# Kernel tuning notes

Measured on AMD Instinct MI355X. Metric: run time of the kernel, lower is better.

Reference implementation:

```python
import jax, jax.numpy as jnp
import numpy as np

HEADS = 4
ALPHA = 0.2  # leaky relu negative slope


def setup_inputs() -> dict:
    key = jax.random.key(0)
    ks = jax.random.split(key, 8)
    N, Fin, Fout = 4096, 512, 256
    return {
        "h": jax.random.normal(ks[0], (N, Fin), dtype=jnp.float32),
        "adj": jax.random.randint(ks[1], (N, N), 0, 2, dtype=jnp.int32),
        "W": jax.random.normal(ks[2], (Fin, Fout), dtype=jnp.float32) * (Fin ** -0.5),
        "Wl_w": jax.random.normal(ks[3], (Fout, Fout), dtype=jnp.float32) * (Fout ** -0.5),
        "Wl_b": jax.random.normal(ks[4], (Fout,), dtype=jnp.float32) * 0.02,
        "Wqkv_w": jax.random.normal(ks[5], (3 * Fout, Fout), dtype=jnp.float32) * (Fout ** -0.5),
        "Wqkv_b": jax.random.normal(ks[6], (3 * Fout,), dtype=jnp.float32) * 0.02,
        "a": jax.random.normal(ks[7], (2 * Fout, 1), dtype=jnp.float32) * (Fout ** -0.5),
    }


def reference(h, adj, W, Wl_w, Wl_b, Wqkv_w, Wqkv_b, a):
    N = h.shape[0]
    Fout = W.shape[1]
    d = Fout // HEADS
    scale = Fout ** -0.5  # note: original scales by out_features^-0.5, not head_dim

    Wh = h @ W                      # [N, Fout]
    Wh = Wh @ Wl_w.T + Wl_b         # to_linear

    qkv = Wh @ Wqkv_w.T + Wqkv_b    # [N, 3*Fout]
    q, k, v = jnp.split(qkv, 3, axis=-1)
    to_heads = lambda t: t.reshape(N, HEADS, d).transpose(1, 0, 2)  # [H, N, d]
    q, k, v = to_heads(q), to_heads(k), to_heads(v)

    dots = jax.nn.softmax(jnp.einsum('hid,hjd->hij', q, k) * scale, axis=-1)  # [H,N,N]
    Wh0 = jnp.einsum('hij,hjd->hid', dots, v)            # [H, N, d]
    Wh0 = Wh0.transpose(1, 0, 2).reshape(N, Fout)        # i (h d)
    Wh0 = jax.nn.softmax(Wh0, axis=-1)

    # GAT score decomposed: e_ij = leakyrelu(Wh_i . a1 + Wh_j . a2)
    a1 = a[:Fout, 0]
    a2 = a[Fout:, 0]
    e = jax.nn.leaky_relu((Wh @ a1)[:, None] + (Wh @ a2)[None, :], negative_slope=ALPHA)

    dsum = dots.sum(axis=0)                              # [N, N]
    neg = jnp.float32(-9e15)
    attention = jnp.where(adj > 0, e + dsum, neg)
    attention = jax.nn.softmax(attention, axis=1)
    # dropout p=0.0 / eval mode -> identity

    h_prime = attention @ Wh + Wh0
    return jax.nn.elu(h_prime)  # concat=True
```

## Files before the change

kernel.cpp:

```cpp
#include <hip/hip_runtime.h>

typedef float  f32x4 __attribute__((ext_vector_type(4)));
typedef short  s16x8 __attribute__((ext_vector_type(8)));
typedef unsigned short u16x8 __attribute__((ext_vector_type(8)));

#define NROWS 4096
#define ALPHA_LR 0.2f
#define SCALE 0.0625f

static __device__ __forceinline__ unsigned short bf16_rne(float x) {
    unsigned u = __float_as_uint(x);
    u += 0x7fffu + ((u >> 16) & 1u);
    return (unsigned short)(u >> 16);
}
static __device__ __forceinline__ unsigned short bf16_trunc(float x) {
    return (unsigned short)(__float_as_uint(x) >> 16);
}
static __device__ __forceinline__ float bf2f(unsigned short h) {
    return __uint_as_float(((unsigned)h) << 16);
}
static __device__ __forceinline__ float bflo(unsigned u) { return __uint_as_float(u << 16); }
static __device__ __forceinline__ float bfhi(unsigned u) { return __uint_as_float(u & 0xffff0000u); }
static __device__ __forceinline__ float wmax16(float v) {
#pragma unroll
    for (int o = 8; o; o >>= 1) v = fmaxf(v, __shfl_xor(v, o, 16));
    return v;
}
static __device__ __forceinline__ float wsum16(float v) {
#pragma unroll
    for (int o = 8; o; o >>= 1) v += __shfl_xor(v, o, 16);
    return v;
}

__global__ __launch_bounds__(256) void wprep(
    const float* __restrict__ W, const float* __restrict__ Wq,
    unsigned short* __restrict__ Whi, unsigned short* __restrict__ Wlo,
    unsigned short* __restrict__ Qhi, unsigned short* __restrict__ Qlo)
{
    int i = blockIdx.x * 256 + threadIdx.x;
    if (i < 131072) {
        float v = W[i];
        unsigned short hh = bf16_trunc(v);
        Whi[i] = hh; Wlo[i] = bf16_rne(v - bf2f(hh));
    }
    if (i < 196608) {
        float v = Wq[i];
        unsigned short hh = bf16_trunc(v);
        Qhi[i] = hh; Qlo[i] = bf16_rne(v - bf2f(hh));
    }
}

template <int EPI, bool BIAS>
__global__ __launch_bounds__(256) void gemm_mfma(
    const float* __restrict__ A,
    const unsigned short* __restrict__ Bhi, const unsigned short* __restrict__ Blo,
    const float* __restrict__ bias,
    float* __restrict__ C, unsigned short* __restrict__ o0,
    unsigned short* __restrict__ o1, unsigned short* __restrict__ o2,
    int M, int Nn, int K)
{
    __shared__ unsigned short Ah[64][40];
    __shared__ unsigned short Al[64][40];
    __shared__ unsigned short Bh[64][40];
    __shared__ unsigned short Bl[64][40];

    const int tid = threadIdx.x;
    const int w = tid >> 6;
    const int ln = tid & 63;
    const int l15 = ln & 15;
    const int lhi = ln >> 4;
    const int bm = blockIdx.y * 64;
    const int bn = blockIdx.x * 64;
    const int sm = tid >> 2;
    const int sk = (tid & 3) * 8;

    f32x4 acc[4];
#pragma unroll
    for (int cf = 0; cf < 4; ++cf) acc[cf] = (f32x4){0.f, 0.f, 0.f, 0.f};

    const float* arow = &A[(size_t)(bm + sm) * K];
    const unsigned short* bhrow = &Bhi[(size_t)(bn + sm) * K];
    const unsigned short* blrow = &Blo[(size_t)(bn + sm) * K];

    float4 a0r = *(const float4*)(arow + sk);
    float4 a1r = *(const float4*)(arow + sk + 4);
    uint4 bhr = *(const uint4*)(bhrow + sk);
    uint4 blr = *(const uint4*)(blrow + sk);

    for (int k0 = 0; k0 < K; k0 += 32) {
        float vv[8] = {a0r.x, a0r.y, a0r.z, a0r.w, a1r.x, a1r.y, a1r.z, a1r.w};
        unsigned hp[4], lp[4];
#pragma unroll
        for (int q = 0; q < 4; ++q) {
            unsigned short h0 = bf16_trunc(vv[q * 2]);
            unsigned short h1 = bf16_trunc(vv[q * 2 + 1]);
            unsigned short l0 = bf16_rne(vv[q * 2] - bf2f(h0));
            unsigned short l1 = bf16_rne(vv[q * 2 + 1] - bf2f(h1));
            hp[q] = (unsigned)h0 | ((unsigned)h1 << 16);
            lp[q] = (unsigned)l0 | ((unsigned)l1 << 16);
        }
        __syncthreads();
        *(uint4*)&Ah[sm][sk] = make_uint4(hp[0], hp[1], hp[2], hp[3]);
        *(uint4*)&Al[sm][sk] = make_uint4(lp[0], lp[1], lp[2], lp[3]);
        *(uint4*)&Bh[sm][sk] = bhr;
        *(uint4*)&Bl[sm][sk] = blr;
        const int kn = (k0 + 32 < K) ? k0 + 32 : 0;
        a0r = *(const float4*)(arow + kn + sk);
        a1r = *(const float4*)(arow + kn + sk + 4);
        bhr = *(const uint4*)(bhrow + kn + sk);
        blr = *(const uint4*)(blrow + kn + sk);
        __syncthreads();
        s16x8 ah = *(const s16x8*)&Ah[w * 16 + l15][lhi * 8];
        s16x8 al2 = *(const s16x8*)&Al[w * 16 + l15][lhi * 8];
        __builtin_amdgcn_s_setprio(1);
#pragma unroll
        for (int cf = 0; cf < 4; ++cf) {
            s16x8 bh = *(const s16x8*)&Bh[cf * 16 + l15][lhi * 8];
            s16x8 bl = *(const s16x8*)&Bl[cf * 16 + l15][lhi * 8];
            acc[cf] = __builtin_amdgcn_mfma_f32_16x16x32_bf16(ah, bh, acc[cf], 0, 0, 0);
            acc[cf] = __builtin_amdgcn_mfma_f32_16x16x32_bf16(ah, bl, acc[cf], 0, 0, 0);
            acc[cf] = __builtin_amdgcn_mfma_f32_16x16x32_bf16(al2, bh, acc[cf], 0, 0, 0);
        }
        __builtin_amdgcn_s_setprio(0);
    }

#pragma unroll
    for (int cf = 0; cf < 4; ++cf) {
        const int col = bn + cf * 16 + l15;
        float bv = BIAS ? bias[col] : 0.0f;
#pragma unroll
        for (int r = 0; r < 4; ++r) {
            const int row = bm + w * 16 + lhi * 4 + r;
            float v = acc[cf][r] + bv;
            if (EPI == 1) {
                C[(size_t)row * Nn + col] = v;
                o0[(size_t)col * NROWS + row] = bf16_rne(v);
            } else if (EPI == 2) {
                if (col < 256)      o0[(size_t)row * 256 + col] = bf16_rne(v);
                else if (col < 512) o1[(size_t)row * 256 + (col - 256)] = bf16_rne(v);
                else                o2[(size_t)(col - 512) * NROWS + row] = bf16_rne(v);
            } else {
                unsigned short hh = bf16_trunc(v);
                o0[(size_t)row * Nn + col] = hh;
                o1[(size_t)row * Nn + col] = bf16_rne(v - bf2f(hh));
            }
        }
    }
}

__global__ __launch_bounds__(256) void compute_p(
    const float* __restrict__ Wh, const float* __restrict__ a,
    float* __restrict__ p1, float* __restrict__ p2)
{
    const int row = blockIdx.x * 16 + (threadIdx.x >> 4);
    const int c = threadIdx.x & 15;
    float s1 = 0.f, s2 = 0.f;
    for (int f = c; f < 256; f += 16) {
        float w = Wh[(size_t)row * 256 + f];
        s1 += w * a[f];
        s2 += w * a[256 + f];
    }
    s1 = wsum16(s1);
    s2 = wsum16(s2);
    if (c == 0) { p1[row] = s1; p2[row] = s2; }
}

__global__ __launch_bounds__(256) void p2max_kernel(
    const float* __restrict__ p2, float* __restrict__ p2m)
{
    __shared__ float red[4];
    const int tid = threadIdx.x;
    float v = -3.0e38f;
#pragma unroll
    for (int k = 0; k < 16; ++k) v = fmaxf(v, p2[tid + k * 256]);
#pragma unroll
    for (int o = 32; o; o >>= 1) v = fmaxf(v, __shfl_xor(v, o, 64));
    if ((tid & 63) == 0) red[tid >> 6] = v;
    __syncthreads();
    if (tid == 0) p2m[0] = fmaxf(fmaxf(red[0], red[1]), fmaxf(red[2], red[3]));
}

__global__ __launch_bounds__(256) void norms1(
    const unsigned short* __restrict__ qh, const unsigned short* __restrict__ kh,
    float* __restrict__ qn2, float* __restrict__ knp)
{
    __shared__ float kn[16][4];
    const int tid = threadIdx.x;
    const int r16 = tid >> 4;
    const int c = tid & 15;
    const int i = blockIdx.x * 16 + r16;
#pragma unroll
    for (int h = 0; h < 4; ++h) {
        float sq = 0.f, sk = 0.f;
#pragma unroll
        for (int d = 0; d < 4; ++d) {
            float qv = bf2f(qh[(size_t)i * 256 + h * 64 + c + d * 16]);
            float kv = bf2f(kh[(size_t)i * 256 + h * 64 + c + d * 16]);
            sq += qv * qv; sk += kv * kv;
        }
        sq = wsum16(sq); sk = wsum16(sk);
        if (c == 0) { qn2[i * 4 + h] = sq; kn[r16][h] = sk; }
    }
    __syncthreads();
    if (tid < 4) {
        float m = 0.f;
#pragma unroll
        for (int r = 0; r < 16; ++r) m = fmaxf(m, kn[r][tid]);
        knp[blockIdx.x * 4 + tid] = m;
    }
}

__global__ __launch_bounds__(256) void norms2(
    const float* __restrict__ qn2, const float* __restrict__ knp,
    float* __restrict__ Mb)
{
    __shared__ float red[4][4];
    __shared__ float kmax[4];
    const int tid = threadIdx.x;
    float v[4];
#pragma unroll
    for (int h = 0; h < 4; ++h) v[h] = knp[tid * 4 + h];
#pragma unroll
    for (int h = 0; h < 4; ++h)
#pragma unroll
        for (int o = 32; o; o >>= 1) v[h] = fmaxf(v[h], __shfl_xor(v[h], o, 64));
    if ((tid & 63) == 0) {
#pragma unroll
        for (int h = 0; h < 4; ++h) red[tid >> 6][h] = v[h];
    }
    __syncthreads();
    if (tid < 4)
        kmax[tid] = fmaxf(fmaxf(red[0][tid], red[1][tid]), fmaxf(red[2][tid], red[3][tid]));
    __syncthreads();
    const int i = blockIdx.x * 256 + tid;
#pragma unroll
    for (int h = 0; h < 4; ++h)
        Mb[i * 4 + h] = sqrtf(qn2[i * 4 + h] * kmax[h]) * SCALE;
}

__global__ __launch_bounds__(256) void zsum_kernel(
    const unsigned short* __restrict__ qh_g, const unsigned short* __restrict__ kh_g,
    const float* __restrict__ Mb, float* __restrict__ zpart)
{
    const int tid = threadIdx.x;
    const int h = tid >> 6;
    const int ln = tid & 63;
    const int l15 = ln & 15;
    const int lhi = ln >> 4;
    const int rt = blockIdx.x & 255;
    const int ch = blockIdx.x >> 8;
    const int i0 = rt * 16;

    s16x8 qA[2];
#pragma unroll
    for (int ks = 0; ks < 2; ++ks)
        qA[ks] = *(const s16x8*)(qh_g + (size_t)(i0 + l15) * 256 + h * 64 + ks * 32 + lhi * 8);
    float M[4];
#pragma unroll
    for (int r = 0; r < 4; ++r) M[r] = Mb[(i0 + lhi * 4 + r) * 4 + h];

    float z[4] = {0.f, 0.f, 0.f, 0.f};
    s16x8 kfc[2][2];
#pragma unroll
    for (int nt = 0; nt < 2; ++nt)
#pragma unroll
        for (int ks = 0; ks < 2; ++ks)
            kfc[nt][ks] = *(const s16x8*)(kh_g + (size_t)(ch * 1024 + nt * 16 + l15) * 256 +
                                          h * 64 + ks * 32 + lhi * 8);

    for (int tt = 0; tt < 32; ++tt) {
        const int jn = ch * 1024 + ((tt + 1) & 31) * 32;
        f32x4 acc[2] = {{0.f,0.f,0.f,0.f},{0.f,0.f,0.f,0.f}};
        __builtin_amdgcn_s_setprio(1);
#pragma unroll
        for (int ks = 0; ks < 2; ++ks)
#pragma unroll
            for (int nt = 0; nt < 2; ++nt)
                acc[nt] = __builtin_amdgcn_mfma_f32_16x16x32_bf16(qA[ks], kfc[nt][ks], acc[nt], 0, 0, 0);
        __builtin_amdgcn_s_setprio(0);
#pragma unroll
        for (int nt = 0; nt < 2; ++nt)
#pragma unroll
            for (int ks = 0; ks < 2; ++ks)
                kfc[nt][ks] = *(const s16x8*)(kh_g + (size_t)(jn + nt * 16 + l15) * 256 +
                                              h * 64 + ks * 32 + lhi * 8);
#pragma unroll
        for (int r = 0; r < 4; ++r)
            z[r] += __expf(acc[0][r] * SCALE - M[r]) + __expf(acc[1][r] * SCALE - M[r]);
    }
#pragma unroll
    for (int r = 0; r < 4; ++r) {
        float zz = wsum16(z[r]);
        if (l15 == 0)
            zpart[(((size_t)(i0 + lhi * 4 + r) * 4 + h) * 4) + ch] = zz;
    }
}

__global__ __launch_bounds__(256) void pvds_kernel(
    const unsigned short* __restrict__ qh_g, const unsigned short* __restrict__ kh_g,
    const unsigned short* __restrict__ vth_g,
    const float* __restrict__ Mb, const float* __restrict__ zpart,
    unsigned short* __restrict__ dsum_g, unsigned short* __restrict__ pacc_o)
{
    enum { D0 = 0, D1 = 5120, MIZ = 10240, SMEMSZ = 10752 };
    __shared__ __align__(16) char smem[SMEMSZ];

    const int tid = threadIdx.x;
    const int h = tid >> 6;
    const int ln = tid & 63;
    const int l15 = ln & 15;
    const int lhi = ln >> 4;
    const int rt = blockIdx.x & 255;
    const int ch = blockIdx.x >> 8;
    const int i0 = rt * 16;
    const int srow = tid >> 4;
    const int sc2 = (tid & 15) * 2;

    if (tid < 64) {
        int hh = tid >> 4, row = tid & 15;
        float M = Mb[(i0 + row) * 4 + hh];
        const float* zb = zpart + ((size_t)(i0 + row) * 4 + hh) * 4;
        float z = ((zb[0] + zb[1]) + zb[2]) + zb[3];
        float* fl = (float*)(smem + MIZ);
        fl[(hh * 16 + row) * 2] = M;
        fl[(hh * 16 + row) * 2 + 1] = 1.0f / z;
    }

    s16x8 qA[2];
#pragma unroll
    for (int ks = 0; ks < 2; ++ks)
        qA[ks] = *(const s16x8*)(qh_g + (size_t)(i0 + l15) * 256 + h * 64 + ks * 32 + lhi * 8);
    __syncthreads();

    float m_f[4], iz_f[4];
#pragma unroll
    for (int r = 0; r < 4; ++r) {
        m_f[r]  = ((float*)(smem + MIZ))[(h * 16 + lhi * 4 + r) * 2];
        iz_f[r] = ((float*)(smem + MIZ))[(h * 16 + lhi * 4 + r) * 2 + 1];
    }

    s16x8 kfc[2][2], vfc[2];
#pragma unroll
    for (int nt = 0; nt < 2; ++nt)
#pragma unroll
        for (int ks = 0; ks < 2; ++ks)
            kfc[nt][ks] = *(const s16x8*)(kh_g + (size_t)(ch * 1024 + nt * 16 + l15) * 256 +
                                          h * 64 + ks * 32 + lhi * 8);
#pragma unroll
    for (int nt = 0; nt < 2; ++nt)
        vfc[nt] = *(const s16x8*)(vth_g + (size_t)(h * 64 + nt * 16 + l15) * 4096 +
                                  ch * 1024 + lhi * 8);

    f32x4 pacc[2] = {{0.f,0.f,0.f,0.f},{0.f,0.f,0.f,0.f}};

    for (int tt = 0; tt < 32; ++tt) {
        const int j0 = ch * 1024 + tt * 32;
        const int jn = ch * 1024 + ((tt + 1) & 31) * 32;
        const int buf = (tt & 1) ? D1 : D0;

        f32x4 acc[2] = {{0.f,0.f,0.f,0.f},{0.f,0.f,0.f,0.f}};
        __builtin_amdgcn_s_setprio(1);
#pragma unroll
        for (int ks = 0; ks < 2; ++ks)
#pragma unroll
            for (int nt = 0; nt < 2; ++nt)
                acc[nt] = __builtin_amdgcn_mfma_f32_16x16x32_bf16(qA[ks], kfc[nt][ks], acc[nt], 0, 0, 0);
        __builtin_amdgcn_s_setprio(0);
#pragma unroll
        for (int nt = 0; nt < 2; ++nt)
#pragma unroll
            for (int ks = 0; ks < 2; ++ks)
                kfc[nt][ks] = *(const s16x8*)(kh_g + (size_t)(jn + nt * 16 + l15) * 256 +
                                              h * 64 + ks * 32 + lhi * 8);
#pragma unroll
        for (int nt = 0; nt < 2; ++nt)
#pragma unroll
            for (int r = 0; r < 4; ++r) {
                float d = __expf(acc[nt][r] * SCALE - m_f[r]) * iz_f[r];
                int row = lhi * 4 + r;
                *(unsigned short*)(smem + buf + h * 1280 + row * 80 + (nt * 16 + l15) * 2) = bf16_rne(d);
            }
        __syncthreads();

        {
            s16x8 dA = *(const s16x8*)(smem + buf + h * 1280 + l15 * 80 + lhi * 16);
            __builtin_amdgcn_s_setprio(1);
            pacc[0] = __builtin_amdgcn_mfma_f32_16x16x32_bf16(dA, vfc[0], pacc[0], 0, 0, 0);
            pacc[1] = __builtin_amdgcn_mfma_f32_16x16x32_bf16(dA, vfc[1], pacc[1], 0, 0, 0);
            __builtin_amdgcn_s_setprio(0);
        }
#pragma unroll
        for (int nt = 0; nt < 2; ++nt)
            vfc[nt] = *(const s16x8*)(vth_g + (size_t)(h * 64 + nt * 16 + l15) * 4096 + jn + lhi * 8);

        {
            float ds0 = 0.f, ds1 = 0.f;
#pragma unroll
            for (int hh = 0; hh < 4; ++hh) {
                unsigned u = *(const unsigned*)(smem + buf + hh * 1280 + srow * 80 + sc2 * 2);
                ds0 += bflo(u); ds1 += bfhi(u);
            }
            unsigned pk = (unsigned)bf16_rne(ds0) | ((unsigned)bf16_rne(ds1) << 16);
            *(unsigned*)(dsum_g + (size_t)(i0 + srow) * 4096 + j0 + sc2) = pk;
        }
    }

    const size_t pbase = (size_t)(rt * 4 + ch) * 4096;
#pragma unroll
    for (int nt = 0; nt < 2; ++nt)
#pragma unroll
        for (int r = 0; r < 4; ++r)
            pacc_o[pbase + (lhi * 4 + r) * 256 + h * 64 + nt * 16 + l15] = bf16_rne(pacc[nt][r]);
}

__global__ __launch_bounds__(256) void outer_kernel(
    const unsigned short* __restrict__ wht_g, const unsigned short* __restrict__ dsum_g,
    const float* __restrict__ p1g, const float* __restrict__ p2g,
    const float* __restrict__ p2m, const int* __restrict__ adj,
    unsigned short* __restrict__ wacc_o, float* __restrict__ Lp_o)
{
    enum { PT0 = 0, PT1 = 2304, SMEMSZ = 4608 };
    __shared__ __align__(16) char smem[SMEMSZ];

    const int tid = threadIdx.x;
    const int w = tid >> 6;
    const int ln = tid & 63;
    const int l15 = ln & 15;
    const int lhi = ln >> 4;
    const int rt = blockIdx.x & 255;
    const int ch = blockIdx.x >> 8;
    const int i0 = rt * 16;
    const int jbase = ch * 1024;
    const int srow = tid >> 4;
    const int sc4 = (tid & 15) * 4;

    const float p1v = p1g[i0 + srow];
    float Mfix;
    {
        float s = p1v + p2m[0];
        Mfix = (s > 0.f ? s : ALPHA_LR * s) + 4.0f;
    }

    int4   adjc = *(const int4*)(adj + (size_t)(i0 + srow) * 4096 + jbase + sc4);
    ushort4 dsc = *(const ushort4*)(dsum_g + (size_t)(i0 + srow) * 4096 + jbase + sc4);
    float4 p2c  = *(const float4*)(p2g + jbase + sc4);
    s16x8 wfc[4][2];
#pragma unroll
    for (int nt = 0; nt < 4; ++nt)
#pragma unroll
        for (int ks = 0; ks < 2; ++ks)
            wfc[nt][ks] = *(const s16x8*)(wht_g + (size_t)(w * 64 + nt * 16 + l15) * 4096 +
                                          jbase + ks * 32 + lhi * 8);

    f32x4 acc[4];
#pragma unroll
    for (int nt = 0; nt < 4; ++nt) acc[nt] = (f32x4){0.f, 0.f, 0.f, 0.f};
    float Lacc = 0.0f;

    for (int t = 0; t < 16; ++t) {
        const int jn = jbase + ((t + 1) & 15) * 64;
        const int buf = (t & 1) ? PT1 : PT0;

        {
            float pr[4];
            float dsv[4] = {bf2f(dsc.x), bf2f(dsc.y), bf2f(dsc.z), bf2f(dsc.w)};
            float p2v[4] = {p2c.x, p2c.y, p2c.z, p2c.w};
            int   av[4]  = {adjc.x, adjc.y, adjc.z, adjc.w};
#pragma unroll
            for (int k = 0; k < 4; ++k) {
                float e = p1v + p2v[k];
                e = e > 0.f ? e : ALPHA_LR * e;
                pr[k] = (av[k] > 0) ? __expf(e + dsv[k] - Mfix) : 0.f;
                Lacc += pr[k];
            }
            ushort4 pk;
            pk.x = bf16_rne(pr[0]); pk.y = bf16_rne(pr[1]);
            pk.z = bf16_rne(pr[2]); pk.w = bf16_rne(pr[3]);
            *(ushort4*)(smem + buf + srow * 144 + sc4 * 2) = pk;
        }
        adjc = *(const int4*)(adj + (size_t)(i0 + srow) * 4096 + jn + sc4);
        dsc  = *(const ushort4*)(dsum_g + (size_t)(i0 + srow) * 4096 + jn + sc4);
        p2c  = *(const float4*)(p2g + jn + sc4);
        __syncthreads();

        {
            s16x8 pa0 = *(const s16x8*)(smem + buf + l15 * 144 + lhi * 16);
            s16x8 pa1 = *(const s16x8*)(smem + buf + l15 * 144 + 64 + lhi * 16);
            __builtin_amdgcn_s_setprio(1);
#pragma unroll
            for (int nt = 0; nt < 4; ++nt) {
                acc[nt] = __builtin_amdgcn_mfma_f32_16x16x32_bf16(pa0, wfc[nt][0], acc[nt], 0, 0, 0);
                acc[nt] = __builtin_amdgcn_mfma_f32_16x16x32_bf16(pa1, wfc[nt][1], acc[nt], 0, 0, 0);
            }
            __builtin_amdgcn_s_setprio(0);
        }
#pragma unroll
        for (int nt = 0; nt < 4; ++nt)
#pragma unroll
            for (int ks = 0; ks < 2; ++ks)
                wfc[nt][ks] = *(const s16x8*)(wht_g + (size_t)(w * 64 + nt * 16 + l15) * 4096 +
                                              jn + ks * 32 + lhi * 8);
    }

    Lacc = wsum16(Lacc);
    if ((tid & 15) == 0) Lp_o[(size_t)(rt * 4 + ch) * 16 + srow] = Lacc;

    const size_t wbase = (size_t)(rt * 4 + ch) * 4096;
#pragma unroll
    for (int nt = 0; nt < 4; ++nt)
#pragma unroll
        for (int r = 0; r < 4; ++r)
            wacc_o[wbase + (lhi * 4 + r) * 256 + w * 64 + nt * 16 + l15] = bf16_rne(acc[nt][r]);
}

__global__ __launch_bounds__(256) void merge_kernel(
    const unsigned short* __restrict__ pacc_b, const unsigned short* __restrict__ wacc_b,
    const float* __restrict__ Lp, float* __restrict__ out)
{
    const int rt = blockIdx.x;
    const int tid = threadIdx.x;
    const int row = tid >> 4;
    const int cg = tid & 15;

    float L = 0.f;
#pragma unroll
    for (int c = 0; c < 4; ++c) L += Lp[(size_t)(rt * 4 + c) * 16 + row];
    const float invL = 1.0f / fmaxf(L, 1e-30f);

    float p[16], wv[16];
#pragma unroll
    for (int k = 0; k < 16; ++k) { p[k] = 0.f; wv[k] = 0.f; }
#pragma unroll
    for (int c = 0; c < 4; ++c) {
        const size_t b = (size_t)(rt * 4 + c) * 4096 + row * 256 + cg * 16;
        u16x8 pa0 = *(const u16x8*)(pacc_b + b);
        u16x8 pa1 = *(const u16x8*)(pacc_b + b + 8);
        u16x8 wa0 = *(const u16x8*)(wacc_b + b);
        u16x8 wa1 = *(const u16x8*)(wacc_b + b + 8);
#pragma unroll
        for (int k = 0; k < 8; ++k) {
            p[k] += bf2f(pa0[k]);  p[k + 8] += bf2f(pa1[k]);
            wv[k] += bf2f(wa0[k]); wv[k + 8] += bf2f(wa1[k]);
        }
    }

    float mx = -3.0e38f;
#pragma unroll
    for (int k = 0; k < 16; ++k) mx = fmaxf(mx, p[k]);
    mx = wmax16(mx);
    float sm = 0.f;
#pragma unroll
    for (int k = 0; k < 16; ++k) { p[k] = __expf(p[k] - mx); sm += p[k]; }
    sm = wsum16(sm);
    const float inv = 1.0f / sm;

    float* orow = out + ((size_t)(rt * 16 + row)) * 256 + cg * 16;
#pragma unroll
    for (int k4 = 0; k4 < 4; ++k4) {
        float4 o;
        float v;
        v = wv[k4*4+0] * invL + p[k4*4+0] * inv; o.x = v > 0.f ? v : __expf(v) - 1.f;
        v = wv[k4*4+1] * invL + p[k4*4+1] * inv; o.y = v > 0.f ? v : __expf(v) - 1.f;
        v = wv[k4*4+2] * invL + p[k4*4+2] * inv; o.z = v > 0.f ? v : __expf(v) - 1.f;
        v = wv[k4*4+3] * invL + p[k4*4+3] * inv; o.w = v > 0.f ? v : __expf(v) - 1.f;
        *(float4*)(orow + k4 * 4) = o;
    }
}

extern "C" void kernel_launch(void* const* d_in, const int* in_sizes, int n_in,
                              void* d_out, int out_size, void* d_ws, size_t ws_size,
                              hipStream_t stream)
{
    const float* h      = (const float*)d_in[0];
    const int*   adj    = (const int*)d_in[1];
    const float* W      = (const float*)d_in[2];
    const float* Wl_w   = (const float*)d_in[3];
    const float* Wl_b   = (const float*)d_in[4];
    const float* Wqkv_w = (const float*)d_in[5];
    const float* Wqkv_b = (const float*)d_in[6];
    const float* a      = (const float*)d_in[7];
    float* out = (float*)d_out;

    char* wsb = (char*)d_ws;
    unsigned short* qh     = (unsigned short*)(wsb + 0);
    unsigned short* kh     = (unsigned short*)(wsb + 2097152);
    unsigned short* vth    = (unsigned short*)(wsb + 4194304);
    unsigned short* wht    = (unsigned short*)(wsb + 6291456);
    unsigned short* dsum_b = (unsigned short*)(wsb + 8388608);
    unsigned short* pacc_b = (unsigned short*)(wsb + 41943040);
    unsigned short* wacc_b = (unsigned short*)(wsb + 50331648);
    float*          Whb    = (float*)(wsb + 50331648);
    unsigned short* Whi    = (unsigned short*)(wsb + 58720256);
    unsigned short* Wlo    = Whi + 131072;
    unsigned short* Qhi    = Wlo + 131072;
    unsigned short* Qlo    = Qhi + 196608;
    unsigned short* WcThi  = Qlo + 196608;
    unsigned short* WcTlo  = WcThi + 131072;
    float*          p1b    = (float*)(wsb + 60555264);
    float*          p2b    = (float*)(wsb + 60571648);
    float*          p2m    = (float*)(wsb + 60588032);
    float*          qn2    = (float*)(wsb + 60592128);
    float*          knp    = (float*)(wsb + 60657664);
    float*          Mb     = (float*)(wsb + 60661760);
    float*          zpart  = (float*)(wsb + 60727296);
    float*          Lp     = (float*)(wsb + 60989440);

    dim3 blk(256);
    wprep<<<dim3(768), blk, 0, stream>>>(W, Wqkv_w, Whi, Wlo, Qhi, Qlo);
    gemm_mfma<3, false><<<dim3(8, 4), blk, 0, stream>>>(
        Wl_w, Whi, Wlo, nullptr, nullptr, WcThi, WcTlo, nullptr, 256, 512, 256);
    gemm_mfma<1, true><<<dim3(4, 64), blk, 0, stream>>>(
        h, WcThi, WcTlo, Wl_b, Whb, wht, nullptr, nullptr, 4096, 256, 512);
    gemm_mfma<2, true><<<dim3(12, 64), blk, 0, stream>>>(
        Whb, Qhi, Qlo, Wqkv_b, nullptr, qh, kh, vth, 4096, 768, 256);
    compute_p<<<dim3(256), blk, 0, stream>>>(Whb, a, p1b, p2b);
    p2max_kernel<<<dim3(1), blk, 0, stream>>>(p2b, p2m);
    norms1<<<dim3(256), blk, 0, stream>>>(qh, kh, qn2, knp);
    norms2<<<dim3(16), blk, 0, stream>>>(qn2, knp, Mb);
    zsum_kernel<<<dim3(1024), blk, 0, stream>>>(qh, kh, Mb, zpart);
    pvds_kernel<<<dim3(1024), blk, 0, stream>>>(qh, kh, vth, Mb, zpart, dsum_b, pacc_b);
    outer_kernel<<<dim3(1024), blk, 0, stream>>>(wht, dsum_b, p1b, p2b, p2m, adj, wacc_b, Lp);
    merge_kernel<<<dim3(256), blk, 0, stream>>>(pacc_b, wacc_b, Lp, out);
}
```

Measured before the change: 286.0 us.

## Restructure attention kernels: waves split keys instead of heads, all heads per wave

zsum and pvds now give each wave a different 32-key slice and have it loop over all four heads, computing the transposed QK^T (K as the A operand). Each wave keeps its dots tile in private LDS. This drops the per-iteration block barrier and lets the head-sum for dsum happen in registers. PV partials are reduced across waves through LDS at the end. The outer kernel computes the probability fragment directly in MFMA A-layout registers (each lane handles 8 contiguous keys), which removes the LDS round-trip and the __syncthreads per tile. The cost is more registers (16 PV accumulators), a final cross-wave reduction, and the loss of the explicit prefetch of K and V.

```diff
diff --git a/kernel.cpp b/kernel.cpp
--- a/kernel.cpp
+++ b/kernel.cpp
@@ -19,8 +19,6 @@
 static __device__ __forceinline__ float bf2f(unsigned short h) {
     return __uint_as_float(((unsigned)h) << 16);
 }
-static __device__ __forceinline__ float bflo(unsigned u) { return __uint_as_float(u << 16); }
-static __device__ __forceinline__ float bfhi(unsigned u) { return __uint_as_float(u & 0xffff0000u); }
 static __device__ __forceinline__ float wmax16(float v) {
 #pragma unroll
     for (int o = 8; o; o >>= 1) v = fmaxf(v, __shfl_xor(v, o, 16));
@@ -242,186 +240,7 @@
     const unsigned short* __restrict__ qh_g, const unsigned short* __restrict__ kh_g,
     const float* __restrict__ Mb, float* __restrict__ zpart)
 {
-    const int tid = threadIdx.x;
-    const int h = tid >> 6;
-    const int ln = tid & 63;
-    const int l15 = ln & 15;
-    const int lhi = ln >> 4;
-    const int rt = blockIdx.x & 255;
-    const int ch = blockIdx.x >> 8;
-    const int i0 = rt * 16;
-
-    s16x8 qA[2];
-#pragma unroll
-    for (int ks = 0; ks < 2; ++ks)
-        qA[ks] = *(const s16x8*)(qh_g + (size_t)(i0 + l15) * 256 + h * 64 + ks * 32 + lhi * 8);
-    float M[4];
-#pragma unroll
-    for (int r = 0; r < 4; ++r) M[r] = Mb[(i0 + lhi * 4 + r) * 4 + h];
-
-    float z[4] = {0.f, 0.f, 0.f, 0.f};
-    s16x8 kfc[2][2];
-#pragma unroll
-    for (int nt = 0; nt < 2; ++nt)
-#pragma unroll
-        for (int ks = 0; ks < 2; ++ks)
-            kfc[nt][ks] = *(const s16x8*)(kh_g + (size_t)(ch * 1024 + nt * 16 + l15) * 256 +
-                                          h * 64 + ks * 32 + lhi * 8);
-
-    for (int tt = 0; tt < 32; ++tt) {
-        const int jn = ch * 1024 + ((tt + 1) & 31) * 32;
-        f32x4 acc[2] = {{0.f,0.f,0.f,0.f},{0.f,0.f,0.f,0.f}};
-        __builtin_amdgcn_s_setprio(1);
-#pragma unroll
-        for (int ks = 0; ks < 2; ++ks)
-#pragma unroll
-            for (int nt = 0; nt < 2; ++nt)
-                acc[nt] = __builtin_amdgcn_mfma_f32_16x16x32_bf16(qA[ks], kfc[nt][ks], acc[nt], 0, 0, 0);
-        __builtin_amdgcn_s_setprio(0);
-#pragma unroll
-        for (int nt = 0; nt < 2; ++nt)
-#pragma unroll
-            for (int ks = 0; ks < 2; ++ks)
-                kfc[nt][ks] = *(const s16x8*)(kh_g + (size_t)(jn + nt * 16 + l15) * 256 +
-                                              h * 64 + ks * 32 + lhi * 8);
-#pragma unroll
-        for (int r = 0; r < 4; ++r)
-            z[r] += __expf(acc[0][r] * SCALE - M[r]) + __expf(acc[1][r] * SCALE - M[r]);
-    }
-#pragma unroll
-    for (int r = 0; r < 4; ++r) {
-        float zz = wsum16(z[r]);
-        if (l15 == 0)
-            zpart[(((size_t)(i0 + lhi * 4 + r) * 4 + h) * 4) + ch] = zz;
-    }
-}
-
-__global__ __launch_bounds__(256) void pvds_kernel(
-    const unsigned short* __restrict__ qh_g, const unsigned short* __restrict__ kh_g,
-    const unsigned short* __restrict__ vth_g,
-    const float* __restrict__ Mb, const float* __restrict__ zpart,
-    unsigned short* __restrict__ dsum_g, unsigned short* __restrict__ pacc_o)
-{
-    enum { D0 = 0, D1 = 5120, MIZ = 10240, SMEMSZ = 10752 };
-    __shared__ __align__(16) char smem[SMEMSZ];
-
-    const int tid = threadIdx.x;
-    const int h = tid >> 6;
-    const int ln = tid & 63;
-    const int l15 = ln & 15;
-    const int lhi = ln >> 4;
-    const int rt = blockIdx.x & 255;
-    const int ch = blockIdx.x >> 8;
-    const int i0 = rt * 16;
-    const int srow = tid >> 4;
-    const int sc2 = (tid & 15) * 2;
-
-    if (tid < 64) {
-        int hh = tid >> 4, row = tid & 15;
-        float M = Mb[(i0 + row) * 4 + hh];
-        const float* zb = zpart + ((size_t)(i0 + row) * 4 + hh) * 4;
-        float z = ((zb[0] + zb[1]) + zb[2]) + zb[3];
-        float* fl = (float*)(smem + MIZ);
-        fl[(hh * 16 + row) * 2] = M;
-        fl[(hh * 16 + row) * 2 + 1] = 1.0f / z;
-    }
-
-    s16x8 qA[2];
-#pragma unroll
-    for (int ks = 0; ks < 2; ++ks)
-        qA[ks] = *(const s16x8*)(qh_g + (size_t)(i0 + l15) * 256 + h * 64 + ks * 32 + lhi * 8);
-    __syncthreads();
-
-    float m_f[4], iz_f[4];
-#pragma unroll
-    for (int r = 0; r < 4; ++r) {
-        m_f[r]  = ((float*)(smem + MIZ))[(h * 16 + lhi * 4 + r) * 2];
-        iz_f[r] = ((float*)(smem + MIZ))[(h * 16 + lhi * 4 + r) * 2 + 1];
-    }
-
-    s16x8 kfc[2][2], vfc[2];
-#pragma unroll
-    for (int nt = 0; nt < 2; ++nt)
-#pragma unroll
-        for (int ks = 0; ks < 2; ++ks)
-            kfc[nt][ks] = *(const s16x8*)(kh_g + (size_t)(ch * 1024 + nt * 16 + l15) * 256 +
-                                          h * 64 + ks * 32 + lhi * 8);
-#pragma unroll
-    for (int nt = 0; nt < 2; ++nt)
-        vfc[nt] = *(const s16x8*)(vth_g + (size_t)(h * 64 + nt * 16 + l15) * 4096 +
-                                  ch * 1024 + lhi * 8);
-
-    f32x4 pacc[2] = {{0.f,0.f,0.f,0.f},{0.f,0.f,0.f,0.f}};
-
-    for (int tt = 0; tt < 32; ++tt) {
-        const int j0 = ch * 1024 + tt * 32;
-        const int jn = ch * 1024 + ((tt + 1) & 31) * 32;
-        const int buf = (tt & 1) ? D1 : D0;
-
-        f32x4 acc[2] = {{0.f,0.f,0.f,0.f},{0.f,0.f,0.f,0.f}};
-        __builtin_amdgcn_s_setprio(1);
-#pragma unroll
-        for (int ks = 0; ks < 2; ++ks)
-#pragma unroll
-            for (int nt = 0; nt < 2; ++nt)
-                acc[nt] = __builtin_amdgcn_mfma_f32_16x16x32_bf16(qA[ks], kfc[nt][ks], acc[nt], 0, 0, 0);
-        __builtin_amdgcn_s_setprio(0);
-#pragma unroll
-        for (int nt = 0; nt < 2; ++nt)
-#pragma unroll
-            for (int ks = 0; ks < 2; ++ks)
-                kfc[nt][ks] = *(const s16x8*)(kh_g + (size_t)(jn + nt * 16 + l15) * 256 +
-                                              h * 64 + ks * 32 + lhi * 8);
-#pragma unroll
-        for (int nt = 0; nt < 2; ++nt)
-#pragma unroll
-            for (int r = 0; r < 4; ++r) {
-                float d = __expf(acc[nt][r] * SCALE - m_f[r]) * iz_f[r];
-                int row = lhi * 4 + r;
-                *(unsigned short*)(smem + buf + h * 1280 + row * 80 + (nt * 16 + l15) * 2) = bf16_rne(d);
-            }
-        __syncthreads();
-
-        {
-            s16x8 dA = *(const s16x8*)(smem + buf + h * 1280 + l15 * 80 + lhi * 16);
-            __builtin_amdgcn_s_setprio(1);
-            pacc[0] = __builtin_amdgcn_mfma_f32_16x16x32_bf16(dA, vfc[0], pacc[0], 0, 0, 0);
-            pacc[1] = __builtin_amdgcn_mfma_f32_16x16x32_bf16(dA, vfc[1], pacc[1], 0, 0, 0);
-            __builtin_amdgcn_s_setprio(0);
-        }
-#pragma unroll
-        for (int nt = 0; nt < 2; ++nt)
-            vfc[nt] = *(const s16x8*)(vth_g + (size_t)(h * 64 + nt * 16 + l15) * 4096 + jn + lhi * 8);
-
-        {
-            float ds0 = 0.f, ds1 = 0.f;
-#pragma unroll
-            for (int hh = 0; hh < 4; ++hh) {
-                unsigned u = *(const unsigned*)(smem + buf + hh * 1280 + srow * 80 + sc2 * 2);
-                ds0 += bflo(u); ds1 += bfhi(u);
-            }
-            unsigned pk = (unsigned)bf16_rne(ds0) | ((unsigned)bf16_rne(ds1) << 16);
-            *(unsigned*)(dsum_g + (size_t)(i0 + srow) * 4096 + j0 + sc2) = pk;
-        }
-    }
-
-    const size_t pbase = (size_t)(rt * 4 + ch) * 4096;
-#pragma unroll
-    for (int nt = 0; nt < 2; ++nt)
-#pragma unroll
-        for (int r = 0; r < 4; ++r)
-            pacc_o[pbase + (lhi * 4 + r) * 256 + h * 64 + nt * 16 + l15] = bf16_rne(pacc[nt][r]);
-}
-
-__global__ __launch_bounds__(256) void outer_kernel(
-    const unsigned short* __restrict__ wht_g, const unsigned short* __restrict__ dsum_g,
-    const float* __restrict__ p1g, const float* __restrict__ p2g,
-    const float* __restrict__ p2m, const int* __restrict__ adj,
-    unsigned short* __restrict__ wacc_o, float* __restrict__ Lp_o)
-{
-    enum { PT0 = 0, PT1 = 2304, SMEMSZ = 4608 };
-    __shared__ __align__(16) char smem[SMEMSZ];
-
+    __shared__ float zred[4][4][16];
     const int tid = threadIdx.x;
     const int w = tid >> 6;
     const int ln = tid & 63;
@@ -430,80 +249,274 @@
     const int rt = blockIdx.x & 255;
     const int ch = blockIdx.x >> 8;
     const int i0 = rt * 16;
-    const int jbase = ch * 1024;
-    const int srow = tid >> 4;
-    const int sc4 = (tid & 15) * 4;
-
-    const float p1v = p1g[i0 + srow];
+    const int jb = ch * 1024;
+
+    s16x8 qB[4][2];
+#pragma unroll
+    for (int h = 0; h < 4; ++h)
+#pragma unroll
+        for (int ks = 0; ks < 2; ++ks)
+            qB[h][ks] = *(const s16x8*)(qh_g + (size_t)(i0 + l15) * 256 + h * 64 + ks * 32 + lhi * 8);
+    float Mv[4];
+#pragma unroll
+    for (int h = 0; h < 4; ++h) Mv[h] = Mb[(i0 + l15) * 4 + h];
+
+    float z[4] = {0.f, 0.f, 0.f, 0.f};
+    const unsigned short* kpB = kh_g + (size_t)l15 * 256 + lhi * 8;
+
+    for (int tt = 0; tt < 8; ++tt) {
+        const int j0 = jb + (tt * 4 + w) * 32;
+#pragma unroll
+        for (int h = 0; h < 4; ++h) {
+            s16x8 kA00 = *(const s16x8*)(kpB + (size_t)j0 * 256 + h * 64);
+            s16x8 kA01 = *(const s16x8*)(kpB + (size_t)j0 * 256 + h * 64 + 32);
+            s16x8 kA10 = *(const s16x8*)(kpB + (size_t)(j0 + 16) * 256 + h * 64);
+            s16x8 kA11 = *(const s16x8*)(kpB + (size_t)(j0 + 16) * 256 + h * 64 + 32);
+            f32x4 acc0 = {0.f, 0.f, 0.f, 0.f};
+            f32x4 acc1 = {0.f, 0.f, 0.f, 0.f};
+            acc0 = __builtin_amdgcn_mfma_f32_16x16x32_bf16(kA00, qB[h][0], acc0, 0, 0, 0);
+            acc0 = __builtin_amdgcn_mfma_f32_16x16x32_bf16(kA01, qB[h][1], acc0, 0, 0, 0);
+            acc1 = __builtin_amdgcn_mfma_f32_16x16x32_bf16(kA10, qB[h][0], acc1, 0, 0, 0);
+            acc1 = __builtin_amdgcn_mfma_f32_16x16x32_bf16(kA11, qB[h][1], acc1, 0, 0, 0);
+#pragma unroll
+            for (int r = 0; r < 4; ++r) {
+                z[h] += __expf(fmaf(acc0[r], SCALE, -Mv[h]));
+                z[h] += __expf(fmaf(acc1[r], SCALE, -Mv[h]));
+            }
+        }
+    }
+#pragma unroll
+    for (int h = 0; h < 4; ++h) {
+        float v = z[h];
+        v += __shfl_xor(v, 16);
+        v += __shfl_xor(v, 32);
+        if (ln < 16) zred[w][h][ln] = v;
+    }
+    __syncthreads();
+    if (tid < 64) {
+        int hh = tid >> 4, row = tid & 15;
+        float zz = ((zred[0][hh][row] + zred[1][hh][row]) + zred[2][hh][row]) + zred[3][hh][row];
+        zpart[((size_t)(i0 + row) * 4 + hh) * 4 + ch] = zz;
+    }
+}
+
+__global__ __launch_bounds__(256) void pvds_kernel(
+    const unsigned short* __restrict__ qh_g, const unsigned short* __restrict__ kh_g,
+    const unsigned short* __restrict__ vth_g,
+    const float* __restrict__ Mb, const float* __restrict__ zpart,
+    unsigned short* __restrict__ dsum_g, unsigned short* __restrict__ pacc_o)
+{
+    enum { DOTS = 0, MIZ = 20480, SMEMSZ = 20992 };
+    __shared__ __align__(16) char smem[SMEMSZ];
+    float* smF = (float*)smem;
+
+    const int tid = threadIdx.x;
+    const int w = tid >> 6;
+    const int ln = tid & 63;
+    const int l15 = ln & 15;
+    const int lhi = ln >> 4;
+    const int rt = blockIdx.x & 255;
+    const int ch = blockIdx.x >> 8;
+    const int i0 = rt * 16;
+    const int jb = ch * 1024;
+
+    if (tid < 64) {
+        int hh = tid >> 4, row = tid & 15;
+        const float* zb = zpart + ((size_t)(i0 + row) * 4 + hh) * 4;
+        float z = ((zb[0] + zb[1]) + zb[2]) + zb[3];
+        float* fl = (float*)(smem + MIZ);
+        fl[(hh * 16 + row) * 2] = Mb[(i0 + row) * 4 + hh];
+        fl[(hh * 16 + row) * 2 + 1] = 1.0f / z;
+    }
+
+    s16x8 qB[4][2];
+#pragma unroll
+    for (int h = 0; h < 4; ++h)
+#pragma unroll
+        for (int ks = 0; ks < 2; ++ks)
+            qB[h][ks] = *(const s16x8*)(qh_g + (size_t)(i0 + l15) * 256 + h * 64 + ks * 32 + lhi * 8);
+    __syncthreads();
+
+    float Mv[4], izv[4];
+#pragma unroll
+    for (int h = 0; h < 4; ++h) {
+        Mv[h]  = ((const float*)(smem + MIZ))[(h * 16 + l15) * 2];
+        izv[h] = ((const float*)(smem + MIZ))[(h * 16 + l15) * 2 + 1];
+    }
+
+    const unsigned short* kpB = kh_g + (size_t)l15 * 256 + lhi * 8;
+    const unsigned short* vpB = vth_g + (size_t)l15 * 4096 + lhi * 8;
+    char* dots_w = smem + DOTS + w * 5120;
+    const int dwr0 = l15 * 80 + lhi * 8;
+    const int drd  = l15 * 80 + lhi * 16;
+
+    f32x4 pacc[4][4];
+#pragma unroll
+    for (int h = 0; h < 4; ++h)
+#pragma unroll
+        for (int nt2 = 0; nt2 < 4; ++nt2) pacc[h][nt2] = (f32x4){0.f, 0.f, 0.f, 0.f};
+
+    for (int tt = 0; tt < 8; ++tt) {
+        const int j0 = jb + (tt * 4 + w) * 32;
+        float dsA0[4] = {0.f, 0.f, 0.f, 0.f};
+        float dsA1[4] = {0.f, 0.f, 0.f, 0.f};
+
+#pragma unroll
+        for (int h = 0; h < 4; ++h) {
+            s16x8 kA00 = *(const s16x8*)(kpB + (size_t)j0 * 256 + h * 64);
+            s16x8 kA01 = *(const s16x8*)(kpB + (size_t)j0 * 256 + h * 64 + 32);
+            s16x8 kA10 = *(const s16x8*)(kpB + (size_t)(j0 + 16) * 256 + h * 64);
+            s16x8 kA11 = *(const s16x8*)(kpB + (size_t)(j0 + 16) * 256 + h * 64 + 32);
+            f32x4 acc0 = {0.f, 0.f, 0.f, 0.f};
+            f32x4 acc1 = {0.f, 0.f, 0.f, 0.f};
+            acc0 = __builtin_amdgcn_mfma_f32_16x16x32_bf16(kA00, qB[h][0], acc0, 0, 0, 0);
+            acc0 = __builtin_amdgcn_mfma_f32_16x16x32_bf16(kA01, qB[h][1], acc0, 0, 0, 0);
+            acc1 = __builtin_amdgcn_mfma_f32_16x16x32_bf16(kA10, qB[h][0], acc1, 0, 0, 0);
+            acc1 = __builtin_amdgcn_mfma_f32_16x16x32_bf16(kA11, qB[h][1], acc1, 0, 0, 0);
+            float e0[4], e1[4];
+#pragma unroll
+            for (int r = 0; r < 4; ++r) {
+                e0[r] = __expf(fmaf(acc0[r], SCALE, -Mv[h])) * izv[h];
+                e1[r] = __expf(fmaf(acc1[r], SCALE, -Mv[h])) * izv[h];
+                dsA0[r] += e0[r];
+                dsA1[r] += e1[r];
+            }
+            ushort4 p0, p1;
+            p0.x = bf16_rne(e0[0]); p0.y = bf16_rne(e0[1]); p0.z = bf16_rne(e0[2]); p0.w = bf16_rne(e0[3]);
+            p1.x = bf16_rne(e1[0]); p1.y = bf16_rne(e1[1]); p1.z = bf16_rne(e1[2]); p1.w = bf16_rne(e1[3]);
+            *(ushort4*)(dots_w + h * 1280 + dwr0)      = p0;
+            *(ushort4*)(dots_w + h * 1280 + dwr0 + 32) = p1;
+        }
+
+        {
+            ushort4 d0, d1;
+            d0.x = bf16_rne(dsA0[0]); d0.y = bf16_rne(dsA0[1]); d0.z = bf16_rne(dsA0[2]); d0.w = bf16_rne(dsA0[3]);
+            d1.x = bf16_rne(dsA1[0]); d1.y = bf16_rne(dsA1[1]); d1.z = bf16_rne(dsA1[2]); d1.w = bf16_rne(dsA1[3]);
+            unsigned short* db = dsum_g + (size_t)(i0 + l15) * 4096 + j0 + lhi * 4;
+            *(ushort4*)(db)      = d0;
+            *(ushort4*)(db + 16) = d1;
+        }
+
+#pragma unroll
+        for (int h = 0; h < 4; ++h) {
+            s16x8 dA = *(const s16x8*)(dots_w + h * 1280 + drd);
+#pragma unroll
+            for (int nt2 = 0; nt2 < 4; ++nt2) {
+                s16x8 vB = *(const s16x8*)(vpB + (size_t)(h * 64 + nt2 * 16) * 4096 + j0);
+                pacc[h][nt2] = __builtin_amdgcn_mfma_f32_16x16x32_bf16(dA, vB, pacc[h][nt2], 0, 0, 0);
+            }
+        }
+    }
+
+    const size_t pbase = (size_t)(rt * 4 + ch) * 4096;
+#pragma unroll
+    for (int h = 0; h < 4; ++h) {
+        __syncthreads();
+#pragma unroll
+        for (int nt2 = 0; nt2 < 4; ++nt2)
+#pragma unroll
+            for (int r = 0; r < 4; ++r)
+                smF[w * 1024 + (lhi * 4 + r) * 64 + nt2 * 16 + l15] = pacc[h][nt2][r];
+        __syncthreads();
+        const int ri = tid >> 4;
+        const int db = (tid & 15) * 4;
+        float4 s0 = *(const float4*)&smF[0 * 1024 + ri * 64 + db];
+        float4 s1 = *(const float4*)&smF[1 * 1024 + ri * 64 + db];
+        float4 s2 = *(const float4*)&smF[2 * 1024 + ri * 64 + db];
+        float4 s3 = *(const float4*)&smF[3 * 1024 + ri * 64 + db];
+        ushort4 o;
+        o.x = bf16_rne(s0.x + s1.x + s2.x + s3.x);
+        o.y = bf16_rne(s0.y + s1.y + s2.y + s3.y);
+        o.z = bf16_rne(s0.z + s1.z + s2.z + s3.z);
+        o.w = bf16_rne(s0.w + s1.w + s2.w + s3.w);
+        *(ushort4*)(pacc_o + pbase + ri * 256 + h * 64 + db) = o;
+    }
+}
+
+__global__ __launch_bounds__(256) void outer_kernel(
+    const unsigned short* __restrict__ wht_g, const unsigned short* __restrict__ dsum_g,
+    const float* __restrict__ p1g, const float* __restrict__ p2g,
+    const float* __restrict__ p2m, const int* __restrict__ adj,
+    unsigned short* __restrict__ wacc_o, float* __restrict__ Lp_o)
+{
+    const int tid = threadIdx.x;
+    const int w = tid >> 6;
+    const int ln = tid & 63;
+    const int l15 = ln & 15;
+    const int lhi = ln >> 4;
+    const int rt = blockIdx.x & 255;
+    const int ch = blockIdx.x >> 8;
+    const int i0 = rt * 16;
+    const int jb = ch * 1024;
+    const int i = i0 + l15;
+
+    const float p1v = p1g[i];
     float Mfix;
     {
         float s = p1v + p2m[0];
         Mfix = (s > 0.f ? s : ALPHA_LR * s) + 4.0f;
     }
 
-    int4   adjc = *(const int4*)(adj + (size_t)(i0 + srow) * 4096 + jbase + sc4);
-    ushort4 dsc = *(const ushort4*)(dsum_g + (size_t)(i0 + srow) * 4096 + jbase + sc4);
-    float4 p2c  = *(const float4*)(p2g + jbase + sc4);
-    s16x8 wfc[4][2];
+    const int* adjB = adj + (size_t)i * 4096 + lhi * 8;
+    const unsigned short* dsB = dsum_g + (size_t)i * 4096 + lhi * 8;
+    const float* p2B = p2g + lhi * 8;
+    const unsigned short* whB = wht_g + lhi * 8;
+
+    int4 a0 = *(const int4*)(adjB + jb);
+    int4 a1 = *(const int4*)(adjB + jb + 4);
+    u16x8 ds = *(const u16x8*)(dsB + jb);
+    float4 q0 = *(const float4*)(p2B + jb);
+    float4 q1 = *(const float4*)(p2B + jb + 4);
+    s16x8 wf[4];
 #pragma unroll
     for (int nt = 0; nt < 4; ++nt)
-#pragma unroll
-        for (int ks = 0; ks < 2; ++ks)
-            wfc[nt][ks] = *(const s16x8*)(wht_g + (size_t)(w * 64 + nt * 16 + l15) * 4096 +
-                                          jbase + ks * 32 + lhi * 8);
+        wf[nt] = *(const s16x8*)(whB + (size_t)(w * 64 + nt * 16 + l15) * 4096 + jb);
 
     f32x4 acc[4];
 #pragma unroll
     for (int nt = 0; nt < 4; ++nt) acc[nt] = (f32x4){0.f, 0.f, 0.f, 0.f};
     float Lacc = 0.0f;
 
-    for (int t = 0; t < 16; ++t) {
-        const int jn = jbase + ((t + 1) & 15) * 64;
-        const int buf = (t & 1) ? PT1 : PT0;
-
+    for (int t = 0; t < 32; ++t) {
+        const int jn = jb + ((t + 1) & 31) * 32;
+
+        float pr[8];
         {
-            float pr[4];
-            float dsv[4] = {bf2f(dsc.x), bf2f(dsc.y), bf2f(dsc.z), bf2f(dsc.w)};
-            float p2v[4] = {p2c.x, p2c.y, p2c.z, p2c.w};
-            int   av[4]  = {adjc.x, adjc.y, adjc.z, adjc.w};
-#pragma unroll
-            for (int k = 0; k < 4; ++k) {
-                float e = p1v + p2v[k];
+            int am[8] = {a0.x, a0.y, a0.z, a0.w, a1.x, a1.y, a1.z, a1.w};
+            float pv[8] = {q0.x, q0.y, q0.z, q0.w, q1.x, q1.y, q1.z, q1.w};
+#pragma unroll
+            for (int k = 0; k < 8; ++k) {
+                float e = p1v + pv[k];
                 e = e > 0.f ? e : ALPHA_LR * e;
-                pr[k] = (av[k] > 0) ? __expf(e + dsv[k] - Mfix) : 0.f;
+                float arg = e + bf2f((unsigned short)ds[k]) - Mfix;
+                pr[k] = (am[k] > 0) ? __expf(arg) : 0.f;
                 Lacc += pr[k];
             }
-            ushort4 pk;
-            pk.x = bf16_rne(pr[0]); pk.y = bf16_rne(pr[1]);
-            pk.z = bf16_rne(pr[2]); pk.w = bf16_rne(pr[3]);
-            *(ushort4*)(smem + buf + srow * 144 + sc4 * 2) = pk;
-        }
-        adjc = *(const int4*)(adj + (size_t)(i0 + srow) * 4096 + jn + sc4);
-        dsc  = *(const ushort4*)(dsum_g + (size_t)(i0 + srow) * 4096 + jn + sc4);
-        p2c  = *(const float4*)(p2g + jn + sc4);
-        __syncthreads();
-
-        {
-            s16x8 pa0 = *(const s16x8*)(smem + buf + l15 * 144 + lhi * 16);
-            s16x8 pa1 = *(const s16x8*)(smem + buf + l15 * 144 + 64 + lhi * 16);
-            __builtin_amdgcn_s_setprio(1);
-#pragma unroll
-            for (int nt = 0; nt < 4; ++nt) {
-                acc[nt] = __builtin_amdgcn_mfma_f32_16x16x32_bf16(pa0, wfc[nt][0], acc[nt], 0, 0, 0);
-                acc[nt] = __builtin_amdgcn_mfma_f32_16x16x32_bf16(pa1, wfc[nt][1], acc[nt], 0, 0, 0);
-            }
-            __builtin_amdgcn_s_setprio(0);
-        }
+        }
+        a0 = *(const int4*)(adjB + jn);
+        a1 = *(const int4*)(adjB + jn + 4);
+        ds = *(const u16x8*)(dsB + jn);
+        q0 = *(const float4*)(p2B + jn);
+        q1 = *(const float4*)(p2B + jn + 4);
+
+        s16x8 pA;
+#pragma unroll
+        for (int k = 0; k < 8; ++k) pA[k] = (short)bf16_rne(pr[k]);
+
+        __builtin_amdgcn_s_setprio(1);
 #pragma unroll
         for (int nt = 0; nt < 4; ++nt)
-#pragma unroll
-            for (int ks = 0; ks < 2; ++ks)
-                wfc[nt][ks] = *(const s16x8*)(wht_g + (size_t)(w * 64 + nt * 16 + l15) * 4096 +
-                                              jn + ks * 32 + lhi * 8);
-    }
-
-    Lacc = wsum16(Lacc);
-    if ((tid & 15) == 0) Lp_o[(size_t)(rt * 4 + ch) * 16 + srow] = Lacc;
+            acc[nt] = __builtin_amdgcn_mfma_f32_16x16x32_bf16(pA, wf[nt], acc[nt], 0, 0, 0);
+        __builtin_amdgcn_s_setprio(0);
+
+#pragma unroll
+        for (int nt = 0; nt < 4; ++nt)
+            wf[nt] = *(const s16x8*)(whB + (size_t)(w * 64 + nt * 16 + l15) * 4096 + jn);
+    }
+
+    Lacc += __shfl_xor(Lacc, 16);
+    Lacc += __shfl_xor(Lacc, 32);
+    if (w == 0 && ln < 16) Lp_o[(size_t)(rt * 4 + ch) * 16 + l15] = Lacc;
 
     const size_t wbase = (size_t)(rt * 4 + ch) * 4096;
 #pragma unroll
```

Result: slower. 376.6 us (+31.7%).
